# Kernel tuning notes

Measured on AMD Instinct MI355X. Metric: run time of the kernel, lower is better.

## Reference

```python
import jax, jax.numpy as jnp
import numpy as np
import itertools

N_BOX = 19
B = 2048
T = 5
_EDGES = np.array(list(itertools.combinations(range(N_BOX), 2)))  # [E,2], E=171
ROW = jnp.asarray(_EDGES[:, 0])
COL = jnp.asarray(_EDGES[:, 1])


def setup_inputs() -> dict:
    key = jax.random.key(0)
    ks = jax.random.split(key, 8)
    return {
        "location_t": jax.random.uniform(ks[0], (B, N_BOX, 5), dtype=jnp.float32),
        "feature_t": jax.random.normal(ks[1], (B, N_BOX, 512), dtype=jnp.float32),
        "mask_t": jax.random.randint(ks[2], (B, N_BOX), 0, 2).astype(bool),
        "past_location_t": jax.random.uniform(ks[3], (B, T, N_BOX, 6), dtype=jnp.float32),
        "W1": jax.random.normal(ks[4], (512, 256), dtype=jnp.float32) * 0.05,
        "b1": jax.random.normal(ks[5], (256,), dtype=jnp.float32) * 0.05,
        "W2": jax.random.normal(ks[6], (256, 512), dtype=jnp.float32) * 0.05,
        "b2": jax.random.normal(ks[7], (512,), dtype=jnp.float32) * 0.05,
    }


def _edge_weights(location_t, mask, past_location_t):
    # bbox centers from cols 1..4: [B,N]
    cx = 0.5 * (location_t[:, :, 1] + location_t[:, :, 3])
    cy = 0.5 * (location_t[:, :, 2] + location_t[:, :, 4])
    d = (cx[:, ROW] - cx[:, COL]) ** 2 + (cy[:, ROW] - cy[:, COL]) ** 2  # [B,E]

    # motion distance, vectorized over all nodes then gathered per edge
    cp = past_location_t[:, :, :, 3:-1] - past_location_t[:, :, :, 1:3]  # [B,T,N,2]
    cpx = cp[..., 0] * 1280.0  # [B,T,N]
    cpy = cp[..., 1] * 720.0
    dx = cpx[:, -1] - cpx[:, 0]  # [B,N]
    dy = cpy[:, -1] - cpy[:, 0]
    length = jnp.sqrt(dx ** 2 + dy ** 2)
    length = jnp.where(length == 0.0, 1.0, length)
    ndx = dx / length
    ndy = dy / length
    x0 = cpx[:, 0]  # [B,N]
    y0 = cpy[:, 0]
    d1 = jnp.sqrt((x0[:, ROW] + ndx[:, ROW] - x0[:, COL] - ndx[:, COL]) ** 2
                  + (y0[:, ROW] + ndy[:, ROW] - y0[:, COL] - ndy[:, COL]) ** 2)
    d2 = jnp.sqrt((x0[:, ROW] - x0[:, COL]) ** 2 + (y0[:, ROW] - y0[:, COL]) ** 2)
    md = d1 - d2  # [B,E]

    w = jnp.exp(-(0.7 * d + 0.3 * md))
    valid = mask[:, ROW] & mask[:, COL]
    w = jnp.where(valid, w, 0.0)
    wmin = jnp.min(w, axis=1, keepdims=True)
    wmax = jnp.max(w, axis=1, keepdims=True)
    return (w - wmin) / (wmax - wmin)


def _gcn(x, ew, W, b):
    # PyG GCNConv: add self loops (weight 1), symmetric normalization, x@W, scatter-add, +bias
    n = x.shape[0]
    loops = jnp.arange(n)
    row = jnp.concatenate([ROW, loops])
    col = jnp.concatenate([COL, loops])
    ew_full = jnp.concatenate([ew, jnp.ones((n,), ew.dtype)])
    deg = jax.ops.segment_sum(ew_full, col, num_segments=n)
    dinv = jnp.where(deg > 0, deg ** -0.5, 0.0)
    norm = dinv[row] * ew_full * dinv[col]  # [E+N]
    xw = x @ W  # [N,F_out]
    out = jnp.zeros((n, W.shape[1]), xw.dtype).at[col].add(norm[:, None] * xw[row])
    return out + b


def reference(location_t, feature_t, mask_t, past_location_t, W1, b1, W2, b2):
    w = _edge_weights(location_t, mask_t, past_location_t)  # [B,E]

    def per_graph(x, ew):
        h = jax.nn.sigmoid(_gcn(x, ew, W1, b1))
        return jax.nn.sigmoid(_gcn(h, ew, W2, b2))

    return jax.vmap(per_graph)(feature_t, w)  # [B,19,512]
```

## Files before the change

### kernel.cpp

```cpp
#include <hip/hip_runtime.h>
#include <hip/hip_bf16.h>
#include <math.h>

#define NBOX 19
#define NEDGE 171
#define TT 5
#define BATCH 2048
#define GB 2
#define MR (GB * NBOX)
#define MP 48

typedef __attribute__((ext_vector_type(8))) short short8v;
typedef __attribute__((ext_vector_type(4))) float f32x4;

static __device__ __forceinline__ ushort f2bf(float f) {
    unsigned int u = __builtin_bit_cast(unsigned int, f);
    return (ushort)((u + 0x8000u) >> 16);
}

static __device__ __forceinline__ float sigm(float x) {
    return __builtin_amdgcn_rcpf(1.0f + __expf(-x));
}

__device__ __forceinline__ int edge_index(int r, int c) {
    return r * (NBOX - 1) - (r * (r - 1)) / 2 + (c - r - 1);
}

__global__ __launch_bounds__(192) void adjpair_kernel(
    const float* __restrict__ loc,
    const int*   __restrict__ mask,
    const float* __restrict__ past,
    ushort* __restrict__ pairimg)
{
    int b = blockIdx.x;
    int p = b >> 1, g = b & 1;
    int tid = threadIdx.x;
    __shared__ float cx[NBOX], cy[NBOX], x0[NBOX], y0[NBOX], ndx[NBOX], ndy[NBOX];
    __shared__ int   mv[NBOX];
    __shared__ float w[NEDGE];
    __shared__ float dinv[NBOX];
    __shared__ float rmn[3], rmx[3];

    if (tid < NBOX) {
        const float* l = loc + ((size_t)b * NBOX + tid) * 5;
        cx[tid] = 0.5f * (l[1] + l[3]);
        cy[tid] = 0.5f * (l[2] + l[4]);
        const float* p0 = past + (((size_t)b * TT + 0) * NBOX + tid) * 6;
        const float* p4 = past + (((size_t)b * TT + (TT - 1)) * NBOX + tid) * 6;
        float cpx0 = (p0[3] - p0[1]) * 1280.0f, cpy0 = (p0[4] - p0[2]) * 720.0f;
        float cpx4 = (p4[3] - p4[1]) * 1280.0f, cpy4 = (p4[4] - p4[2]) * 720.0f;
        float dx = cpx4 - cpx0, dy = cpy4 - cpy0;
        float len = sqrtf(dx * dx + dy * dy);
        if (len == 0.0f) len = 1.0f;
        ndx[tid] = dx / len;
        ndy[tid] = dy / len;
        x0[tid] = cpx0;
        y0[tid] = cpy0;
        mv[tid] = mask[(size_t)b * NBOX + tid];
    }
    __syncthreads();

    float wv = 0.0f;
    if (tid < NEDGE) {
        int rem = tid, rr = 0;
        while (rem >= NBOX - 1 - rr) { rem -= NBOX - 1 - rr; rr++; }
        int r = rr, c = rr + 1 + rem;
        float ddx = cx[r] - cx[c], ddy = cy[r] - cy[c];
        float d = ddx * ddx + ddy * ddy;
        float ax = x0[r] + ndx[r] - x0[c] - ndx[c];
        float ay = y0[r] + ndy[r] - y0[c] - ndy[c];
        float d1 = sqrtf(ax * ax + ay * ay);
        float bx = x0[r] - x0[c], by = y0[r] - y0[c];
        float d2 = sqrtf(bx * bx + by * by);
        float md = d1 - d2;
        wv = expf(-(0.7f * d + 0.3f * md));
        if (!(mv[r] && mv[c])) wv = 0.0f;
    }

    float lmn = (tid < NEDGE) ? wv : INFINITY;
    float lmx = (tid < NEDGE) ? wv : -INFINITY;
#pragma unroll
    for (int o = 32; o; o >>= 1) {
        lmn = fminf(lmn, __shfl_xor(lmn, o));
        lmx = fmaxf(lmx, __shfl_xor(lmx, o));
    }
    if ((tid & 63) == 0) { rmn[tid >> 6] = lmn; rmx[tid >> 6] = lmx; }
    __syncthreads();
    float mn = fminf(rmn[0], fminf(rmn[1], rmn[2]));
    float mx = fmaxf(rmx[0], fmaxf(rmx[1], rmx[2]));
    float inv_range = 1.0f / (mx - mn);
    if (tid < NEDGE) w[tid] = (wv - mn) * inv_range;
    __syncthreads();

    if (tid < NBOX) {
        float s = 1.0f;
        for (int rr = 0; rr < tid; rr++) s += w[edge_index(rr, tid)];
        dinv[tid] = 1.0f / sqrtf(s);
    }
    __syncthreads();

    {
        int row_local = tid >> 3, chunk = tid & 7;
        int row = (g == 0)
            ? (row_local < NBOX ? row_local : NBOX + row_local)
            : (row_local < NBOX ? NBOX + row_local : 24 + row_local);
        ushort vals[8];
#pragma unroll
        for (int i = 0; i < 8; i++) {
            int col = chunk * 8 + i;
            int rc = col - g * NBOX;
            float v = 0.0f;
            if (row_local < NBOX && rc >= 0 && rc < NBOX) {
                int cc = row_local;
                if (rc == cc) v = dinv[cc] * dinv[cc];
                else if (rc < cc) v = w[edge_index(rc, cc)] * dinv[rc] * dinv[cc];
            }
            vals[i] = f2bf(v);
        }
        int boff = (row * 128 + chunk * 16) ^ ((row & 7) << 4);
        *(int4*)((char*)pairimg + (size_t)p * 6144 + boff) = *(int4*)vals;
    }
}

__global__ void packT2_kernel(const float* __restrict__ W1,
                              const float* __restrict__ W2,
                              ushort* __restrict__ W1T,
                              ushort* __restrict__ W2T)
{
    int idx = blockIdx.x * blockDim.x + threadIdx.x;
    if (idx < 131072) {
        int n = idx / 512, k = idx % 512;
        W1T[idx] = f2bf(W1[(size_t)k * 256 + n]);
    } else {
        int j = idx - 131072;
        int n = j / 256, k = j % 256;
        W2T[j] = f2bf(W2[(size_t)k * 512 + n]);
    }
}

__global__ __launch_bounds__(256, 4) void fused_kernel(
    const float*  __restrict__ feat,
    const ushort* __restrict__ pairimg,
    const ushort* __restrict__ W1T,
    const ushort* __restrict__ W2T,
    const float*  __restrict__ b1,
    const float*  __restrict__ b2,
    float* __restrict__ out)
{
    __shared__ __align__(16) ushort XHs[MP * 256];
    __shared__ __align__(16) ushort YsT[64 * 64];
    __shared__ __align__(16) ushort AdjS[MP * 64];

    const int tid = threadIdx.x;
    const int lane = tid & 63, wvi = tid >> 6;
    const int rowbase = blockIdx.x * MR;
    const int ncol = wvi * 16 + (lane & 15);
    const int kgrp = lane >> 4;
    const int l15 = lane & 15;

#pragma unroll
    for (int p = 0; p < 2; p++)
        ((int4*)YsT)[tid + p * 256] = make_int4(0, 0, 0, 0);

    {
        const int4* src = (const int4*)((const char*)pairimg + (size_t)blockIdx.x * 6144);
        ((int4*)AdjS)[tid] = src[tid];
        if (tid < 128) ((int4*)AdjS)[tid + 256] = src[tid + 256];
    }

    f32x4 acc1[4][3];
#pragma unroll
    for (int c = 0; c < 4; c++)
#pragma unroll
        for (int m = 0; m < 3; m++) acc1[c][m] = (f32x4){0.f, 0.f, 0.f, 0.f};

    for (int kh = 0; kh < 2; kh++) {
        __syncthreads();
        const float* fg = feat + (size_t)rowbase * 512 + kh * 256;
#pragma unroll
        for (int p = 0; p < 12; p++) {
            int i = tid + p * 256;
            int row = i >> 6, q = i & 63;
            ushort4 h;
            if (i < MR * 64) {
                float4 v = *(const float4*)(fg + (size_t)row * 512 + q * 4);
                h.x = f2bf(v.x); h.y = f2bf(v.y); h.z = f2bf(v.z); h.w = f2bf(v.w);
            } else {
                h.x = 0; h.y = 0; h.z = 0; h.w = 0;
            }
            int boff = (row * 512 + q * 8) ^ ((row & 7) << 4);
            *(ushort4*)((char*)XHs + boff) = h;
        }
        __syncthreads();

        const ushort* bpb = W1T + (size_t)ncol * 512 + kh * 256 + kgrp * 8;
        short8v br[3][4];
#pragma unroll
        for (int c = 0; c < 4; c++)
            br[0][c] = *(const short8v*)(bpb + (size_t)c * 64 * 512);
#pragma unroll
        for (int c = 0; c < 4; c++)
            br[1][c] = *(const short8v*)(bpb + (size_t)c * 64 * 512 + 32);
#pragma unroll
        for (int ks = 0; ks < 8; ks++) {
            if (ks < 6) {
#pragma unroll
                for (int c = 0; c < 4; c++)
                    br[(ks + 2) % 3][c] =
                        *(const short8v*)(bpb + (size_t)c * 64 * 512 + (ks + 2) * 32);
            }
            short8v a[3];
#pragma unroll
            for (int m = 0; m < 3; m++) {
                int row = m * 16 + l15;
                int boff = (row * 512 + ks * 64 + kgrp * 16) ^ ((row & 7) << 4);
                a[m] = *(const short8v*)((char*)XHs + boff);
            }
#pragma unroll
            for (int c = 0; c < 4; c++)
#pragma unroll
                for (int m = 0; m < 3; m++)
                    acc1[c][m] = __builtin_amdgcn_mfma_f32_16x16x32_bf16(
                        a[m], br[ks % 3][c], acc1[c][m], 0, 0, 0);
        }
    }
    __syncthreads();

#pragma unroll
    for (int c = 0; c < 4; c++) {
#pragma unroll
        for (int m = 0; m < 3; m++) {
            int gr0 = m * 16 + kgrp * 4;
            ushort4 hq;
            hq.x = f2bf(acc1[c][m][0]); hq.y = f2bf(acc1[c][m][1]);
            hq.z = f2bf(acc1[c][m][2]); hq.w = f2bf(acc1[c][m][3]);
            int boff = (ncol * 128 + gr0 * 2) ^ ((ncol & 7) << 4);
            *(ushort4*)((char*)YsT + boff) = hq;
        }
        short8v yb[2];
#pragma unroll
        for (int ks = 0; ks < 2; ks++)
            yb[ks] = *(const short8v*)((char*)YsT +
                     ((ncol * 128 + ks * 64 + kgrp * 16) ^ ((ncol & 7) << 4)));
        float bv = b1[c * 64 + ncol];
#pragma unroll
        for (int mt = 0; mt < 3; mt++) {
            f32x4 o = (f32x4){0.f, 0.f, 0.f, 0.f};
#pragma unroll
            for (int ks = 0; ks < 2; ks++) {
                int ar = mt * 16 + l15;
                short8v af = *(const short8v*)((char*)AdjS +
                             ((ar * 128 + ks * 64 + kgrp * 16) ^ ((ar & 7) << 4)));
                o = __builtin_amdgcn_mfma_f32_16x16x32_bf16(af, yb[ks], o, 0, 0, 0);
            }
#pragma unroll
            for (int j = 0; j < 4; j++) {
                int grp = mt * 16 + kgrp * 4 + j;
                float s = sigm(o[j] + bv);
                int boff = (grp * 512 + (c * 64 + ncol) * 2) ^ ((grp & 7) << 4);
                *(ushort*)((char*)XHs + boff) = f2bf(s);
            }
        }
    }
    __syncthreads();

#pragma unroll 1
    for (int half = 0; half < 2; half++) {
        f32x4 acc[4][3];
#pragma unroll
        for (int c = 0; c < 4; c++)
#pragma unroll
            for (int m = 0; m < 3; m++) acc[c][m] = (f32x4){0.f, 0.f, 0.f, 0.f};

        const ushort* bpb = W2T + (size_t)(half * 256 + ncol) * 256 + kgrp * 8;
        short8v br[3][4];
#pragma unroll
        for (int c = 0; c < 4; c++)
            br[0][c] = *(const short8v*)(bpb + (size_t)c * 64 * 256);
#pragma unroll
        for (int c = 0; c < 4; c++)
            br[1][c] = *(const short8v*)(bpb + (size_t)c * 64 * 256 + 32);
#pragma unroll
        for (int ks = 0; ks < 8; ks++) {
            if (ks < 6) {
#pragma unroll
                for (int c = 0; c < 4; c++)
                    br[(ks + 2) % 3][c] =
                        *(const short8v*)(bpb + (size_t)c * 64 * 256 + (ks + 2) * 32);
            }
            short8v a[3];
#pragma unroll
            for (int m = 0; m < 3; m++) {
                int row = m * 16 + l15;
                int boff = (row * 512 + ks * 64 + kgrp * 16) ^ ((row & 7) << 4);
                a[m] = *(const short8v*)((char*)XHs + boff);
            }
#pragma unroll
            for (int c = 0; c < 4; c++)
#pragma unroll
                for (int m = 0; m < 3; m++)
                    acc[c][m] = __builtin_amdgcn_mfma_f32_16x16x32_bf16(
                        a[m], br[ks % 3][c], acc[c][m], 0, 0, 0);
        }

#pragma unroll
        for (int c = 0; c < 4; c++) {
            int cg = half * 4 + c;
#pragma unroll
            for (int m = 0; m < 3; m++) {
                int gr0 = m * 16 + kgrp * 4;
                ushort4 hq;
                hq.x = f2bf(acc[c][m][0]); hq.y = f2bf(acc[c][m][1]);
                hq.z = f2bf(acc[c][m][2]); hq.w = f2bf(acc[c][m][3]);
                int boff = (ncol * 128 + gr0 * 2) ^ ((ncol & 7) << 4);
                *(ushort4*)((char*)YsT + boff) = hq;
            }
            short8v yb[2];
#pragma unroll
            for (int ks = 0; ks < 2; ks++)
                yb[ks] = *(const short8v*)((char*)YsT +
                         ((ncol * 128 + ks * 64 + kgrp * 16) ^ ((ncol & 7) << 4)));
            float bv = b2[cg * 64 + ncol];
#pragma unroll
            for (int mt = 0; mt < 3; mt++) {
                f32x4 o = (f32x4){0.f, 0.f, 0.f, 0.f};
#pragma unroll
                for (int ks = 0; ks < 2; ks++) {
                    int ar = mt * 16 + l15;
                    short8v af = *(const short8v*)((char*)AdjS +
                                 ((ar * 128 + ks * 64 + kgrp * 16) ^ ((ar & 7) << 4)));
                    o = __builtin_amdgcn_mfma_f32_16x16x32_bf16(af, yb[ks], o, 0, 0, 0);
                }
#pragma unroll
                for (int j = 0; j < 4; j++) {
                    int grp = mt * 16 + kgrp * 4 + j;
                    if (grp < MR) {
                        float s = sigm(o[j] + bv);
                        out[(size_t)(rowbase + grp) * 512 + cg * 64 + ncol] = s;
                    }
                }
            }
        }
    }
}

extern "C" void kernel_launch(void* const* d_in, const int* in_sizes, int n_in,
                              void* d_out, int out_size, void* d_ws, size_t ws_size,
                              hipStream_t stream) {
    const float* loc  = (const float*)d_in[0];
    const float* feat = (const float*)d_in[1];
    const int*   mask = (const int*)d_in[2];
    const float* past = (const float*)d_in[3];
    const float* W1   = (const float*)d_in[4];
    const float* b1   = (const float*)d_in[5];
    const float* W2   = (const float*)d_in[6];
    const float* b2   = (const float*)d_in[7];

    ushort* pairimg = (ushort*)d_ws;
    ushort* W1T     = pairimg + (size_t)(BATCH / 2) * 3072;
    ushort* W2T     = W1T + 256 * 512;

    adjpair_kernel<<<BATCH, 192, 0, stream>>>(loc, mask, past, pairimg);
    packT2_kernel<<<1024, 256, 0, stream>>>(W1, W2, W1T, W2T);

    fused_kernel<<<BATCH / GB, 256, 0, stream>>>(feat, pairimg, W1T, W2T, b1, b2,
                                                 (float*)d_out);
}
```

Measured before the change: 106.9 us.

## Double-buffer feature K-chunks in LDS with register prefetch overlapping MFMA

Splits the first GEMM's K dimension into four 128-wide chunks and stages each into one of two LDS buffers. The next chunk's global loads are issued into registers before the MFMA loop and written to LDS afterwards, so global latency overlaps compute. The padding rows are zeroed once instead of on every pass. In exchange it uses more registers for the prefetched data, which may reduce occupancy, and it adds an extra barrier per chunk.

Result: slower. 113.2 us (+5.9%).

```diff
diff --git a/kernel.cpp b/kernel.cpp
--- a/kernel.cpp
+++ b/kernel.cpp
@@ -158,9 +158,31 @@
     const int kgrp = lane >> 4;
     const int l15 = lane & 15;
 
+    float4 x0p[5];
+    {
+        const float* fg0 = feat + (size_t)rowbase * 512;
+#pragma unroll
+        for (int p = 0; p < 5; p++) {
+            int i = tid + p * 256;
+            if (i < MR * 32) {
+                int row = i >> 5, q32 = i & 31;
+                x0p[p] = *(const float4*)(fg0 + (size_t)row * 512 + q32 * 4);
+            }
+        }
+    }
+
 #pragma unroll
     for (int p = 0; p < 2; p++)
         ((int4*)YsT)[tid + p * 256] = make_int4(0, 0, 0, 0);
+
+    {
+        if (tid < 160) ((int4*)((char*)XHs + 9728))[tid] = make_int4(0, 0, 0, 0);
+        else if (tid < 192)
+            ;
+        int t2 = tid - 64;
+        if (t2 >= 0 && t2 < 160)
+            ((int4*)((char*)XHs + 22016))[t2] = make_int4(0, 0, 0, 0);
+    }
 
     {
         const int4* src = (const int4*)((const char*)pairimg + (size_t)blockIdx.x * 6144);
@@ -168,32 +190,42 @@
         if (tid < 128) ((int4*)AdjS)[tid + 256] = src[tid + 256];
     }
 
+#pragma unroll
+    for (int p = 0; p < 5; p++) {
+        int i = tid + p * 256;
+        if (i < MR * 32) {
+            int row = i >> 5, q32 = i & 31;
+            ushort4 h;
+            h.x = f2bf(x0p[p].x); h.y = f2bf(x0p[p].y);
+            h.z = f2bf(x0p[p].z); h.w = f2bf(x0p[p].w);
+            int boff = (row * 256 + q32 * 8) ^ ((row & 7) << 4);
+            *(ushort4*)((char*)XHs + boff) = h;
+        }
+    }
+    __syncthreads();
+
     f32x4 acc1[4][3];
 #pragma unroll
     for (int c = 0; c < 4; c++)
 #pragma unroll
         for (int m = 0; m < 3; m++) acc1[c][m] = (f32x4){0.f, 0.f, 0.f, 0.f};
 
-    for (int kh = 0; kh < 2; kh++) {
-        __syncthreads();
-        const float* fg = feat + (size_t)rowbase * 512 + kh * 256;
-#pragma unroll
-        for (int p = 0; p < 12; p++) {
-            int i = tid + p * 256;
-            int row = i >> 6, q = i & 63;
-            ushort4 h;
-            if (i < MR * 64) {
-                float4 v = *(const float4*)(fg + (size_t)row * 512 + q * 4);
-                h.x = f2bf(v.x); h.y = f2bf(v.y); h.z = f2bf(v.z); h.w = f2bf(v.w);
-            } else {
-                h.x = 0; h.y = 0; h.z = 0; h.w = 0;
-            }
-            int boff = (row * 512 + q * 8) ^ ((row & 7) << 4);
-            *(ushort4*)((char*)XHs + boff) = h;
-        }
-        __syncthreads();
-
-        const ushort* bpb = W1T + (size_t)ncol * 512 + kh * 256 + kgrp * 8;
+#pragma unroll
+    for (int q = 0; q < 4; q++) {
+        const int qb = (q & 1) * 12288;
+        float4 xp[5];
+        if (q < 3) {
+            const float* fgn = feat + (size_t)rowbase * 512 + (q + 1) * 128;
+#pragma unroll
+            for (int p = 0; p < 5; p++) {
+                int i = tid + p * 256;
+                if (i < MR * 32) {
+                    int row = i >> 5, q32 = i & 31;
+                    xp[p] = *(const float4*)(fgn + (size_t)row * 512 + q32 * 4);
+                }
+            }
+        }
+        const ushort* bpb = W1T + (size_t)ncol * 512 + q * 128 + kgrp * 8;
         short8v br[3][4];
 #pragma unroll
         for (int c = 0; c < 4; c++)
@@ -202,18 +234,18 @@
         for (int c = 0; c < 4; c++)
             br[1][c] = *(const short8v*)(bpb + (size_t)c * 64 * 512 + 32);
 #pragma unroll
-        for (int ks = 0; ks < 8; ks++) {
-            if (ks < 6) {
+        for (int ksq = 0; ksq < 4; ksq++) {
+            if (ksq < 2) {
 #pragma unroll
                 for (int c = 0; c < 4; c++)
-                    br[(ks + 2) % 3][c] =
-                        *(const short8v*)(bpb + (size_t)c * 64 * 512 + (ks + 2) * 32);
+                    br[(ksq + 2) % 3][c] =
+                        *(const short8v*)(bpb + (size_t)c * 64 * 512 + (ksq + 2) * 32);
             }
             short8v a[3];
 #pragma unroll
             for (int m = 0; m < 3; m++) {
                 int row = m * 16 + l15;
-                int boff = (row * 512 + ks * 64 + kgrp * 16) ^ ((row & 7) << 4);
+                int boff = ((row * 256 + ksq * 64 + kgrp * 16) ^ ((row & 7) << 4)) + qb;
                 a[m] = *(const short8v*)((char*)XHs + boff);
             }
 #pragma unroll
@@ -221,10 +253,25 @@
 #pragma unroll
                 for (int m = 0; m < 3; m++)
                     acc1[c][m] = __builtin_amdgcn_mfma_f32_16x16x32_bf16(
-                        a[m], br[ks % 3][c], acc1[c][m], 0, 0, 0);
-        }
-    }
-    __syncthreads();
+                        a[m], br[ksq % 3][c], acc1[c][m], 0, 0, 0);
+        }
+        if (q < 3) {
+            const int nqb = ((q + 1) & 1) * 12288;
+#pragma unroll
+            for (int p = 0; p < 5; p++) {
+                int i = tid + p * 256;
+                if (i < MR * 32) {
+                    int row = i >> 5, q32 = i & 31;
+                    ushort4 h;
+                    h.x = f2bf(xp[p].x); h.y = f2bf(xp[p].y);
+                    h.z = f2bf(xp[p].z); h.w = f2bf(xp[p].w);
+                    int boff = ((row * 256 + q32 * 8) ^ ((row & 7) << 4)) + nqb;
+                    *(ushort4*)((char*)XHs + boff) = h;
+                }
+            }
+        }
+        __syncthreads();
+    }
 
 #pragma unroll
     for (int c = 0; c < 4; c++) {
```
